# Optimization experiments

Hardware: AMD Instinct MI355X
Metric: run time of the kernel (lower is better)

The kernel has to match this reference:

```python
import jax, jax.numpy as jnp
import numpy as np

B, C, H, W = 8, 256, 64, 64
HID = 4 * C          # mlp_ratio = 4
M = C // 8           # KAttention scale = 8
EPS = 1e-6


def setup_inputs() -> dict:
    key = jax.random.key(0)
    ks = jax.random.split(key, 24)
    n = lambda k, s, sc=1.0: jax.random.normal(k, s, dtype=jnp.float32) * sc
    return {
        "x": n(ks[0], (B, C, H, W)),
        "y": n(ks[1], (B, C, H, W)),
        # shared SeparableConvBN(dim, dim, k=3): 1x1 conv -> depthwise 3x3 -> BN(eval, folded to scale/shift)
        "conv_pw_w": n(ks[2], (C, C), 0.05),
        "conv_dw_w": n(ks[3], (C, 1, 3, 3), 0.1),
        "conv_bn_s": 1.0 + n(ks[4], (C,), 0.1),
        "conv_bn_t": n(ks[5], (C,), 0.1),
        # shared BatchNorm2d(dim) `self.norm` (eval mode, folded)
        "norm_s": 1.0 + n(ks[6], (C,), 0.1),
        "norm_t": n(ks[7], (C,), 0.1),
        # KAttention 1x1 convs (no bias) + gamma
        "q_w": n(ks[8], (M, C), 0.05),
        "k_w": n(ks[9], (M, C), 0.05),
        "v_w": n(ks[10], (C, C), 0.05),
        "gamma_k": n(ks[11], (1,), 0.1),
        # CAttention gamma
        "gamma_c": n(ks[12], (1,), 0.1),
        # Mlp: ConvBN(1x1, bias) -> ReLU6 -> ConvBN(1x1, bias); dropout = identity (eval)
        "fc1_w": n(ks[13], (HID, C), 0.05),
        "fc1_b": n(ks[14], (HID,), 0.05),
        "bn1_s": 1.0 + n(ks[15], (HID,), 0.1),
        "bn1_t": n(ks[16], (HID,), 0.1),
        "fc2_w": n(ks[17], (C, HID), 0.05),
        "fc2_b": n(ks[18], (C,), 0.05),
        "bn2_s": 1.0 + n(ks[19], (C,), 0.1),
        "bn2_t": n(ks[20], (C,), 0.1),
    }


def _bn(x, s, t):
    return x * s[None, :, None, None] + t[None, :, None, None]


def _c1(x, w, b=None):
    # 1x1 conv as channel matmul: [B,C,H,W] x [O,C] -> [B,O,H,W]
    out = jnp.einsum('bchw,oc->bohw', x, w)
    return out if b is None else out + b[None, :, None, None]


def _dw3(x, w):
    # depthwise 3x3, padding=1
    return jax.lax.conv_general_dilated(
        x, w, window_strides=(1, 1), padding='SAME',
        feature_group_count=x.shape[1],
        dimension_numbers=('NCHW', 'OIHW', 'NCHW'))


def reference(x, y, conv_pw_w, conv_dw_w, conv_bn_s, conv_bn_t, norm_s, norm_t,
              q_w, k_w, v_w, gamma_k, gamma_c,
              fc1_w, fc1_b, bn1_s, bn1_t, fc2_w, fc2_b, bn2_s, bn2_t):

    def sepconvbn(z):
        return _bn(_dw3(_c1(z, conv_pw_w), conv_dw_w), conv_bn_s, conv_bn_t)

    def norm(z):
        return _bn(z, norm_s, norm_t)

    def katt(z):
        b, c, h, w = z.shape
        N = h * w
        Q = jax.nn.softplus(_c1(z, q_w)).reshape(b, M, N).transpose(0, 2, 1)  # [b,N,m]
        K = jax.nn.softplus(_c1(z, k_w)).reshape(b, M, N)                    # [b,m,N]
        V = _c1(z, v_w).reshape(b, c, N)                                     # [b,c,N]
        KV = jnp.einsum('bmn,bcn->bmc', K, V)                                # [b,m,c]
        inv = 1.0 / jnp.einsum('bnm,bm->bn', Q, K.sum(-1) + EPS)            # [b,N]
        wv = jnp.einsum('bnm,bmc,bn->bcn', Q, KV, inv)                       # [b,c,N]
        return z + gamma_k[0] * wv.reshape(b, c, h, w)

    def catt(z):
        b, c, h, w = z.shape
        f = z.reshape(b, c, h * w)
        energy = jnp.einsum('bcn,bdn->bcd', f, f)                            # [b,c,c]
        att = jax.nn.softmax(energy.max(-1, keepdims=True) - energy, axis=-1)
        out = jnp.einsum('bcd,bdn->bcn', att, f).reshape(b, c, h, w)
        return gamma_c[0] * out + z

    def light(z):
        return katt(z) + catt(z)

    def mlp(z):
        hdn = jnp.clip(_bn(_c1(z, fc1_w, fc1_b), bn1_s, bn1_t), 0.0, 6.0)  # ReLU6
        return _bn(_c1(hdn, fc2_w, fc2_b), bn2_s, bn2_t)

    x1 = norm(sepconvbn(x))
    ax1 = light(x1)
    y1 = norm(sepconvbn(y))
    ay1 = light(y1)
    x2 = mlp(norm(x1 * ay1))
    y2 = mlp(norm(y1 * ax1))
    y3 = y + y2
    x3 = x + x2 + y3
    return (x3, y3)
```

## Files before the change

### kernel.cpp

```cpp
#include <hip/hip_runtime.h>
#include <hip/hip_bf16.h>
#include <math.h>

typedef __hip_bfloat16 bf16;
typedef unsigned short u16;
#define DEV __device__ __forceinline__

DEV float tofl(float v){ return v; }
DEV bf16  f2b(float v){ return __float2bfloat16(v); }
DEV u16   f2bu(float v){ bf16 h = f2b(v); u16 u; __builtin_memcpy(&u,&h,2); return u; }
DEV float u2f(u16 u){ bf16 h; __builtin_memcpy(&h,&u,2); return __bfloat162float(h); }

static constexpr int Cc=256, Nn=4096, Mm=32;
static constexpr size_t ACT = (size_t)8*Cc*Nn;
static constexpr float EPSc = 1e-6f;

typedef __attribute__((ext_vector_type(8))) __bf16 bf16x8;
typedef __attribute__((ext_vector_type(4))) float  f32x4;

struct StageRegs { int4 a[4], b[4]; };

DEV void stage_load(const u16* __restrict__ gA, int ldA,
                    const u16* __restrict__ gB, int ldB, int tid, StageRegs& r)
{
  int row = tid>>3, g = tid&7;
#pragma unroll
  for(int i=0;i<4;i++){
    r.a[i] = *(const int4*)(gA + (size_t)(row+32*i)*ldA + g*8);
    r.b[i] = *(const int4*)(gB + (size_t)(row+32*i)*ldB + g*8);
  }
}
DEV void stage_write(u16* __restrict__ sA, u16* __restrict__ sB,
                     int tid, const StageRegs& r)
{
  int row = tid>>3, g = tid&7;
#pragma unroll
  for(int i=0;i<4;i++){
    int rr = row+32*i;
    int gg = ((g ^ (rr&7))<<3);
    *(int4*)(sA + rr*64 + gg) = r.a[i];
    *(int4*)(sB + rr*64 + gg) = r.b[i];
  }
}

template<int KDIM, int OMODE>
__global__ __launch_bounds__(256,2) void gemm_bf16(
    const u16* __restrict__ A, long sAb,
    const u16* __restrict__ B,
    float* __restrict__ Cf, u16* __restrict__ Cb,
    const float* __restrict__ bia, const float* __restrict__ scl,
    const float* __restrict__ sht)
{
  __shared__ __align__(16) u16 sA[2][8192];
  __shared__ __align__(16) u16 sB[2][8192];
  int tid = threadIdx.x;
  int nt = blockIdx.x, mt = blockIdx.y, b = blockIdx.z;
  const u16* gA = A + (size_t)b*sAb + (size_t)mt*128*KDIM;
  const u16* gB = B + ((size_t)b*4096 + (size_t)nt*128)*KDIM;
  int w = tid>>6, l = tid&63;
  int wr = w>>1, wc = w&1;
  int l15 = l&15, lg = l>>4;
  f32x4 acc[4][4] = {};
  StageRegs r;
  stage_load(gA, KDIM, gB, KDIM, tid, r);
  stage_write(sA[0], sB[0], tid, r);
  __syncthreads();
  constexpr int NT = KDIM/64;
  for(int t=0;t<NT;t++){
    int cur = t&1;
    if(t+1<NT) stage_load(gA + (t+1)*64, KDIM, gB + (t+1)*64, KDIM, tid, r);
#pragma unroll
    for(int ks=0;ks<2;ks++){
      bf16x8 af[4], bfr[4];
#pragma unroll
      for(int m=0;m<4;m++){
        int row = wr*64 + m*16 + l15;
        int g = ks*4 + lg;
        af[m] = *(const bf16x8*)(&sA[cur][row*64 + ((g^(row&7))<<3)]);
      }
#pragma unroll
      for(int nn=0;nn<4;nn++){
        int row = wc*64 + nn*16 + l15;
        int g = ks*4 + lg;
        bfr[nn] = *(const bf16x8*)(&sB[cur][row*64 + ((g^(row&7))<<3)]);
      }
#pragma unroll
      for(int m=0;m<4;m++)
#pragma unroll
        for(int nn=0;nn<4;nn++)
          acc[m][nn] = __builtin_amdgcn_mfma_f32_16x16x32_bf16(af[m], bfr[nn], acc[m][nn], 0,0,0);
    }
    if(t+1<NT) stage_write(sA[cur^1], sB[cur^1], tid, r);
    __syncthreads();
  }
  int obase = mt*128 + wr*64;
  int nbase = nt*128 + wc*64;
  if (OMODE==0){
    size_t Mrows = (size_t)gridDim.y*128;
#pragma unroll
    for(int m=0;m<4;m++)
#pragma unroll
      for(int nn=0;nn<4;nn++){
        int o_ = obase + m*16 + (lg<<2);
        int n_ = nbase + nn*16 + l15;
        float* dst = Cf + (((size_t)b*Mrows + o_)<<12) + n_;
#pragma unroll
        for(int i=0;i<4;i++) dst[(size_t)i<<12] = acc[m][nn][i];
      }
  } else if (OMODE==1){
#pragma unroll
    for(int m=0;m<4;m++)
#pragma unroll
      for(int nn=0;nn<4;nn++){
        int o_ = obase + m*16 + (lg<<2);
        int n_ = nbase + nn*16 + l15;
        union { u16 u[4]; uint2 v; } pk;
#pragma unroll
        for(int i=0;i<4;i++){
          int o = o_+i;
          float a2 = (acc[m][nn][i] + bia[o])*scl[o] + sht[o];
          pk.u[i] = f2bu(fminf(fmaxf(a2,0.f),6.f));
        }
        *(uint2*)(Cb + ((size_t)b*4096 + (size_t)n_)*1024 + o_) = pk.v;
      }
  } else {
    size_t Mrows = (size_t)gridDim.y*128;
#pragma unroll
    for(int m=0;m<4;m++)
#pragma unroll
      for(int nn=0;nn<4;nn++){
        int o_ = obase + m*16 + (lg<<2);
        int n_ = nbase + nn*16 + l15;
        u16* dst = Cb + (((size_t)b*Mrows + o_)<<12) + n_;
#pragma unroll
        for(int i=0;i<4;i++) dst[(size_t)i<<12] = f2bu(acc[m][nn][i]);
      }
  }
}

__global__ __launch_bounds__(256,2) void qk_gemm(
    const u16* __restrict__ Aqk, const u16* __restrict__ B,
    float* __restrict__ Qf, float* __restrict__ Kf, u16* __restrict__ Kb)
{
  __shared__ __align__(16) u16 sA[2][8192];
  __shared__ __align__(16) u16 sB[2][8192];
  int tid = threadIdx.x;
  int nt = blockIdx.x, b = blockIdx.z;
  const u16* gA = Aqk;
  const u16* gB = B + ((size_t)b*4096 + (size_t)nt*128)*256;
  int w = tid>>6, l = tid&63;
  int wr = w>>1, wc = w&1;
  int l15 = l&15, lg = l>>4;
  f32x4 acc[4][4] = {};
  StageRegs r;
  stage_load(gA, 256, gB, 256, tid, r);
  stage_write(sA[0], sB[0], tid, r);
  __syncthreads();
  for(int t=0;t<4;t++){
    int cur = t&1;
    if(t+1<4) stage_load(gA + (t+1)*64, 256, gB + (t+1)*64, 256, tid, r);
#pragma unroll
    for(int ks=0;ks<2;ks++){
      bf16x8 af[4], bfr[4];
#pragma unroll
      for(int m=0;m<4;m++){
        int row = wr*64 + m*16 + l15;
        int g = ks*4 + lg;
        af[m] = *(const bf16x8*)(&sA[cur][row*64 + ((g^(row&7))<<3)]);
      }
#pragma unroll
      for(int nn=0;nn<4;nn++){
        int row = wc*64 + nn*16 + l15;
        int g = ks*4 + lg;
        bfr[nn] = *(const bf16x8*)(&sB[cur][row*64 + ((g^(row&7))<<3)]);
      }
#pragma unroll
      for(int m=0;m<4;m++)
#pragma unroll
        for(int nn=0;nn<4;nn++)
          acc[m][nn] = __builtin_amdgcn_mfma_f32_16x16x32_bf16(af[m], bfr[nn], acc[m][nn], 0,0,0);
    }
    if(t+1<4) stage_write(sA[cur^1], sB[cur^1], tid, r);
    __syncthreads();
  }
  if (wr!=0) return;
  int nbase = nt*128 + wc*64;
#pragma unroll
  for(int m=0;m<4;m++)
#pragma unroll
    for(int nn=0;nn<4;nn++){
      int o_ = m*16 + (lg<<2);
      int n_ = nbase + nn*16 + l15;
#pragma unroll
      for(int i=0;i<4;i++){
        float a = acc[m][nn][i];
        a = fmaxf(a,0.f) + log1pf(expf(-fabsf(a)));
        if (m<2){
          Qf[(((size_t)b*32 + o_+i)<<12) + n_] = a;
        } else {
          int kr = o_+i-32;
          Kf[(((size_t)b*32 + kr)<<12) + n_] = a;
          Kb[(((size_t)b*32 + kr)<<12) + n_] = f2bu(a);
        }
      }
    }
}

__global__ __launch_bounds__(256,2) void kv_gemm(const u16* __restrict__ Kb,
    const u16* __restrict__ Vb, float* __restrict__ Cp)
{
  __shared__ __align__(16) u16 sA[2][8192];
  __shared__ __align__(16) u16 sB[2][8192];
  int tid = threadIdx.x;
  int nt = blockIdx.x;
  int b  = blockIdx.z >> 4, ks = blockIdx.z & 15;
  const u16* gA = Kb + ((size_t)b*32)*4096 + ks*256;
  const u16* gB = Vb + ((size_t)b*256 + (size_t)nt*128)*4096 + ks*256;
  int row = tid>>3, g = tid&7;
  int w = tid>>6, l = tid&63;
  int wr = w>>1, wc = w&1;
  int l15 = l&15, lg = l>>4;
  f32x4 acc[4][4] = {};
  StageRegs r;
#define KV_LOAD(koff) do { \
    _Pragma("unroll") \
    for(int i=0;i<4;i++){ \
      r.a[i] = *(const int4*)(gA + (size_t)row*4096 + (koff) + g*8); \
      r.b[i] = *(const int4*)(gB + (size_t)(row+32*i)*4096 + (koff) + g*8); \
    } } while(0)
  KV_LOAD(0);
  stage_write(sA[0], sB[0], tid, r);
  __syncthreads();
  for(int t=0;t<4;t++){
    int cur = t&1;
    if(t+1<4) KV_LOAD((t+1)*64);
#pragma unroll
    for(int kss=0;kss<2;kss++){
      bf16x8 af[4], bfr[4];
#pragma unroll
      for(int m=0;m<4;m++){
        int rr = wr*64 + m*16 + l15;
        int gg = kss*4 + lg;
        af[m] = *(const bf16x8*)(&sA[cur][rr*64 + ((gg^(rr&7))<<3)]);
      }
#pragma unroll
      for(int nn=0;nn<4;nn++){
        int rr = wc*64 + nn*16 + l15;
        int gg = kss*4 + lg;
        bfr[nn] = *(const bf16x8*)(&sB[cur][rr*64 + ((gg^(rr&7))<<3)]);
      }
#pragma unroll
      for(int m=0;m<4;m++)
#pragma unroll
        for(int nn=0;nn<4;nn++)
          acc[m][nn] = __builtin_amdgcn_mfma_f32_16x16x32_bf16(af[m], bfr[nn], acc[m][nn], 0,0,0);
    }
    if(t+1<4) stage_write(sA[cur^1], sB[cur^1], tid, r);
    __syncthreads();
  }
#undef KV_LOAD
  if (wr!=0) return;
  float* Cb = Cp + ((size_t)ks*8 + b)*8192;
#pragma unroll
  for(int m=0;m<2;m++)
#pragma unroll
    for(int nn=0;nn<4;nn++){
      int o_ = m*16 + (lg<<2);
      int c_ = nt*128 + wc*64 + nn*16 + l15;
#pragma unroll
      for(int i=0;i<4;i++) Cb[(size_t)(o_+i)*256 + c_] = acc[m][nn][i];
    }
}

__global__ __launch_bounds__(256) void kv_combine16(const float* __restrict__ p,
    float* __restrict__ o)
{
  int i = blockIdx.x*256 + threadIdx.x;
  float s = 0.f;
#pragma unroll
  for(int ks=0;ks<16;ks++) s += p[(size_t)ks*65536 + i];
  o[i] = s;
}

template<int KTILES, int KSPLIT, int OMODE>
__global__ __launch_bounds__(256,2) void gemm3(
    const u16* __restrict__ Ah, const u16* __restrict__ Al, int ldA, long sAb,
    const u16* __restrict__ Bh, const u16* __restrict__ Bl, int ldB, long sBb,
    float* __restrict__ Cf)
{
  __shared__ __align__(16) u16 sA[2][8192];
  __shared__ __align__(16) u16 sB[2][8192];
  int tid = threadIdx.x;
  int nt = blockIdx.x, mt = blockIdx.y;
  int b  = blockIdx.z / KSPLIT, ks = blockIdx.z % KSPLIT;
  long koff = (long)ks * (KTILES*64);
  const u16* A0 = Ah + (size_t)b*sAb + (size_t)mt*128*ldA + koff;
  const u16* A1 = Al + (size_t)b*sAb + (size_t)mt*128*ldA + koff;
  const u16* B0 = Bh + (size_t)b*sBb + (size_t)nt*128*ldB + koff;
  const u16* B1 = Bl + (size_t)b*sBb + (size_t)nt*128*ldB + koff;
  int w = tid>>6, l = tid&63;
  int wr = w>>1, wc = w&1;
  int l15 = l&15, lg = l>>4;
  f32x4 acc[4][4] = {};
  StageRegs r;
  for(int pass=0; pass<3; ++pass){
    const u16* gA = (pass==2) ? A1 : A0;
    const u16* gB = (pass==1) ? B1 : B0;
    stage_load(gA, ldA, gB, ldB, tid, r);
    stage_write(sA[0], sB[0], tid, r);
    __syncthreads();
    for(int t=0;t<KTILES;t++){
      int cur = t&1;
      if(t+1<KTILES) stage_load(gA + (t+1)*64, ldA, gB + (t+1)*64, ldB, tid, r);
#pragma unroll
      for(int kss=0;kss<2;kss++){
        bf16x8 af[4], bfr[4];
#pragma unroll
        for(int m=0;m<4;m++){
          int row = wr*64 + m*16 + l15;
          int g = kss*4 + lg;
          af[m] = *(const bf16x8*)(&sA[cur][row*64 + ((g^(row&7))<<3)]);
        }
#pragma unroll
        for(int nn=0;nn<4;nn++){
          int row = wc*64 + nn*16 + l15;
          int g = kss*4 + lg;
          bfr[nn] = *(const bf16x8*)(&sB[cur][row*64 + ((g^(row&7))<<3)]);
        }
#pragma unroll
        for(int m=0;m<4;m++)
#pragma unroll
          for(int nn=0;nn<4;nn++)
            acc[m][nn] = __builtin_amdgcn_mfma_f32_16x16x32_bf16(af[m], bfr[nn], acc[m][nn], 0,0,0);
      }
      if(t+1<KTILES) stage_write(sA[cur^1], sB[cur^1], tid, r);
      __syncthreads();
    }
  }
  int obase = mt*128 + wr*64;
  int nbase = nt*128 + wc*64;
  if (OMODE==0){
    size_t Mrows = (size_t)gridDim.y*128;
#pragma unroll
    for(int m=0;m<4;m++)
#pragma unroll
      for(int nn=0;nn<4;nn++){
        int o_ = obase + m*16 + (lg<<2);
        int n_ = nbase + nn*16 + l15;
        float* dst = Cf + (((size_t)b*Mrows + o_)<<12) + n_;
#pragma unroll
        for(int i=0;i<4;i++) dst[(size_t)i<<12] = acc[m][nn][i];
      }
  } else {
    int gridB = gridDim.z / KSPLIT;
    float* Cb = Cf + ((size_t)ks*gridB + b)*65536;
#pragma unroll
    for(int m=0;m<4;m++)
#pragma unroll
      for(int nn=0;nn<4;nn++){
        int o_ = obase + m*16 + (lg<<2);
        int n_ = nbase + nn*16 + l15;
#pragma unroll
        for(int i=0;i<4;i++) Cb[(size_t)(o_+i)*256 + n_] = acc[m][nn][i];
      }
  }
}

__global__ __launch_bounds__(256) void cvt_w(const float* __restrict__ s,
    u16* __restrict__ d)
{
  int i = blockIdx.x*256 + threadIdx.x;
  d[i] = f2bu(s[i]);
}
__global__ __launch_bounds__(256) void cvt_wsplit(const float* __restrict__ s,
    u16* __restrict__ dh, u16* __restrict__ dl)
{
  int i = blockIdx.x*256 + threadIdx.x;
  float v = s[i];
  u16 h = f2bu(v);
  dh[i] = h; dl[i] = f2bu(v - u2f(h));
}
__global__ __launch_bounds__(256) void cvt_qk(const float* __restrict__ q,
    const float* __restrict__ k, u16* __restrict__ A)
{
  int r = blockIdx.x, c = threadIdx.x;
  float v = 0.f;
  if (r < 32) v = q[r*256 + c];
  else if (r < 64) v = k[(r-32)*256 + c];
  A[r*256 + c] = f2bu(v);
}
__global__ __launch_bounds__(256) void cvt_split_nm(const float* __restrict__ x,
    u16* __restrict__ xh, u16* __restrict__ xl)
{
  int n  = blockIdx.x*256 + threadIdx.x;
  int c0 = blockIdx.y*16;
  int b  = blockIdx.z;
  union { u16 u[16]; uint4 q[2]; } ph, pl;
#pragma unroll
  for (int oo=0;oo<16;oo++){
    float v = x[(((size_t)b*256 + c0 + oo)<<12) + n];
    u16 h = f2bu(v);
    ph.u[oo] = h; pl.u[oo] = f2bu(v - u2f(h));
  }
  size_t o = (((size_t)b*4096 + n)<<8) + c0;
  *(uint4*)(xh+o) = ph.q[0]; *(uint4*)(xh+o+8) = ph.q[1];
  *(uint4*)(xl+o) = pl.q[0]; *(uint4*)(xl+o+8) = pl.q[1];
}
__global__ __launch_bounds__(256) void cvt_transpose(const u16* __restrict__ zc,
    u16* __restrict__ zn)
{
  int n  = blockIdx.x*256 + threadIdx.x;
  int c0 = blockIdx.y*16;
  int b  = blockIdx.z;
  union { u16 u[16]; uint4 q[2]; } pk;
#pragma unroll
  for (int oo=0;oo<16;oo++)
    pk.u[oo] = zc[(((size_t)b*256 + c0 + oo)<<12) + n];
  u16* dst = zn + (((size_t)b*4096 + n)<<8) + c0;
  *(uint4*)dst       = pk.q[0];
  *(uint4*)(dst + 8) = pk.q[1];
}

__global__ __launch_bounds__(256) void dw_norm_tile(const float* __restrict__ pw,
    u16* __restrict__ zh, u16* __restrict__ zl, const float* __restrict__ dww,
    const float* __restrict__ cbs, const float* __restrict__ cbt,
    const float* __restrict__ ns, const float* __restrict__ nt)
{
  int bc = blockIdx.x;
  int c = bc & 255;
  __shared__ float sp[66*66];
  int tid = threadIdx.x;
  if (tid < 66){ sp[tid] = 0.f; sp[65*66 + tid] = 0.f; }
  if (tid >= 128 && tid < 192) sp[(tid-128+1)*66] = 0.f;
  if (tid >= 192)              sp[(tid-192+1)*66 + 65] = 0.f;
  const float* src = pw + ((size_t)bc << 12);
#pragma unroll
  for(int it=0; it<4; it++){
    int idx = tid + it*256;
    int r = idx >> 4, c4 = idx & 15;
    float4 v = *(const float4*)(src + (idx<<2));
    float* d = &sp[(r+1)*66 + 1 + (c4<<2)];
    d[0]=v.x; d[1]=v.y; d[2]=v.z; d[3]=v.w;
  }
  __syncthreads();
  const float* wp = dww + c*9;
  float w00=wp[0], w01=wp[1], w02=wp[2],
        w10=wp[3], w11=wp[4], w12=wp[5],
        w20=wp[6], w21=wp[7], w22=wp[8];
  float sc = cbs[c]*ns[c];
  float sh = cbt[c]*ns[c] + nt[c];
  int r  = tid >> 2;
  int c0 = (tid & 3) << 4;
  const float* row0 = &sp[r*66 + c0];
  const float* row1 = row0 + 66;
  const float* row2 = row1 + 66;
  union { u16 u[16]; uint4 q[2]; } ph, pl;
#pragma unroll
  for(int j=0;j<16;j++){
    float acc = w00*row0[j] + w01*row0[j+1] + w02*row0[j+2]
              + w10*row1[j] + w11*row1[j+1] + w12*row1[j+2]
              + w20*row2[j] + w21*row2[j+1] + w22*row2[j+2];
    float v = acc*sc + sh;
    u16 hi = f2bu(v);
    ph.u[j] = hi; pl.u[j] = f2bu(v - u2f(hi));
  }
  size_t o = ((size_t)bc << 12) + (r<<6) + c0;
  *(uint4*)(zh+o)   = ph.q[0]; *(uint4*)(zh+o+8) = ph.q[1];
  *(uint4*)(zl+o)   = pl.q[0]; *(uint4*)(zl+o+8) = pl.q[1];
}

__global__ __launch_bounds__(256) void softmax16(const float* __restrict__ Ep,
    u16* __restrict__ att)
{
  int bc = blockIdx.x;
  int b = bc>>8, c = bc&255;
  size_t base = (size_t)b*65536 + (size_t)c*256;
  int d = threadIdx.x;
  float ed = 0.f;
#pragma unroll
  for(int ks=0;ks<16;ks++) ed += Ep[base + (size_t)ks*524288 + d];
  __shared__ float red[4];
  int lane = d&63, wid = d>>6;
  float v = ed;
  for (int off=32;off;off>>=1) v = fmaxf(v, __shfl_down(v,off));
  if(lane==0) red[wid]=v;
  __syncthreads();
  float rowmax = fmaxf(fmaxf(red[0],red[1]),fmaxf(red[2],red[3]));
  __syncthreads();
  float s = rowmax - ed;
  float v2 = s;
  for (int off=32;off;off>>=1) v2 = fmaxf(v2, __shfl_down(v2,off));
  if(lane==0) red[wid]=v2;
  __syncthreads();
  float smax = fmaxf(fmaxf(red[0],red[1]),fmaxf(red[2],red[3]));
  __syncthreads();
  float p = expf(s - smax);
  float sv = p;
  for (int off=32;off;off>>=1) sv += __shfl_down(sv,off);
  if(lane==0) red[wid]=sv;
  __syncthreads();
  float sum = red[0]+red[1]+red[2]+red[3];
  att[((size_t)bc<<8)+d] = f2bu(p/sum);
}

__global__ __launch_bounds__(256) void catt_px(const u16* __restrict__ zh,
    const u16* __restrict__ zl, const u16* __restrict__ oh,
    const u16* __restrict__ ol, const float* __restrict__ Qf,
    const float* __restrict__ KVf, const float* __restrict__ invb,
    const u16* __restrict__ s1b, const float* __restrict__ gkp,
    const float* __restrict__ gcp, const float* __restrict__ ns,
    const float* __restrict__ nt, u16* __restrict__ px)
{
  int n  = blockIdx.x*256 + threadIdx.x;
  int c0 = blockIdx.y*16;
  int b  = blockIdx.z;
  const float* qb  = Qf  + (((size_t)b*Mm)<<12) + n;
  const float* kvb = KVf + ((size_t)b<<13) + c0;
  float s2[16] = {};
#pragma unroll
  for (int m=0;m<Mm;m++){
    float qm = qb[(size_t)m<<12];
#pragma unroll
    for (int oo=0;oo<16;oo++) s2[oo] = fmaf(qm, kvb[m*256 + oo], s2[oo]);
  }
  float invv = invb[((size_t)b<<12)+n];
  float gk = gkp[0], gc = gcp[0];
  union { u16 u[16]; uint4 q[2]; } pk;
#pragma unroll
  for (int oo=0;oo<16;oo++){
    int c = c0+oo;
    size_t idx = (((size_t)b*256 + c)<<12) + n;
    float zv = u2f(zh[idx]) + u2f(zl[idx]);
    float ov = u2f(oh[idx]) + u2f(ol[idx]);
    float a = 2.f*zv + gc*u2f(s1b[idx]) + gk*s2[oo]*invv;
    pk.u[oo] = f2bu(ov*a*ns[c] + nt[c]);
  }
  u16* dst = px + (((size_t)b*4096 + n)<<8) + c0;
  *(uint4*)dst       = pk.q[0];
  *(uint4*)(dst + 8) = pk.q[1];
}

__global__ __launch_bounds__(256) void rowsum_lit(const float* __restrict__ A, float* __restrict__ out)
{
  int x = blockIdx.x;
  const float* ar = A + ((size_t)x << 12);
  float a = 0.f;
  for(int n=threadIdx.x; n<Nn; n+=256) a += ar[n];
  __shared__ float red[4];
  for(int off=32;off;off>>=1) a += __shfl_down(a,off);
  int lane = threadIdx.x&63, wid = threadIdx.x>>6;
  if(lane==0) red[wid]=a;
  __syncthreads();
  if(threadIdx.x==0) out[x] = red[0]+red[1]+red[2]+red[3];
}

__global__ __launch_bounds__(256) void inv_lit(const float* __restrict__ Qf,
    const float* __restrict__ Ks, float* __restrict__ invb)
{
  size_t idx = (size_t)blockIdx.x*256 + threadIdx.x;
  int b = (int)(idx>>12);
  const float* qb = Qf + ((size_t)b*Mm << 12) + (int)(idx&4095);
  const float* ks = Ks + b*Mm;
  float s = 0.f;
  for(int m=0;m<Mm;m++) s += qb[(size_t)m<<12]*(ks[m]+EPSc);
  invb[idx] = 1.f/s;
}

__global__ __launch_bounds__(256) void final_y(const float* __restrict__ yin,
    const float* __restrict__ acc, const float* __restrict__ b2,
    const float* __restrict__ s2, const float* __restrict__ t2, float* __restrict__ out)
{
  size_t idx = (size_t)blockIdx.x*256 + threadIdx.x;
  int c = (int)((idx>>12) & 255);
  float y2 = (acc[idx] + b2[c])*s2[c] + t2[c];
  out[ACT + idx] = yin[idx] + y2;
}

__global__ __launch_bounds__(256) void final_x(const float* __restrict__ xin,
    const float* __restrict__ acc, const float* __restrict__ b2,
    const float* __restrict__ s2, const float* __restrict__ t2, float* __restrict__ out)
{
  size_t idx = (size_t)blockIdx.x*256 + threadIdx.x;
  int c = (int)((idx>>12) & 255);
  float x2 = (acc[idx] + b2[c])*s2[c] + t2[c];
  out[idx] = xin[idx] + x2 + out[ACT + idx];
}

extern "C" void kernel_launch(void* const* d_in, const int* in_sizes, int n_in,
                              void* d_out, int out_size, void* d_ws, size_t ws_size,
                              hipStream_t stream)
{
  (void)in_sizes; (void)n_in; (void)out_size; (void)ws_size;
  const float* xin  = (const float*)d_in[0];
  const float* yin  = (const float*)d_in[1];
  const float* pw_w = (const float*)d_in[2];
  const float* dw_w = (const float*)d_in[3];
  const float* cbs  = (const float*)d_in[4];
  const float* cbt  = (const float*)d_in[5];
  const float* ns   = (const float*)d_in[6];
  const float* nt   = (const float*)d_in[7];
  const float* q_w  = (const float*)d_in[8];
  const float* k_w  = (const float*)d_in[9];
  const float* v_w  = (const float*)d_in[10];
  const float* gk   = (const float*)d_in[11];
  const float* gc   = (const float*)d_in[12];
  const float* fc1_w= (const float*)d_in[13];
  const float* fc1_b= (const float*)d_in[14];
  const float* bn1s = (const float*)d_in[15];
  const float* bn1t = (const float*)d_in[16];
  const float* fc2_w= (const float*)d_in[17];
  const float* fc2_b= (const float*)d_in[18];
  const float* bn2s = (const float*)d_in[19];
  const float* bn2t = (const float*)d_in[20];

  char* ws = (char*)d_ws;
  u16*   Vb    = (u16*)  (ws);
  float* KVp   = (float*)(ws + 16777216);
  u16*   Kb    = (u16*)  (ws + 20971520);
  float* Ep    = (float*)(ws);
  u16*   s1b16 = (u16*)  (ws);
  float* accb  = (float*)(ws);
  float* Apw   = (float*)(ws);
  u16*   x1h   = (u16*)  (ws + 33554432);
  u16*   x1l   = (u16*)  (ws + 50331648);
  u16*   y1h   = (u16*)  (ws + 67108864);
  u16*   y1l   = (u16*)  (ws + 83886080);
  u16*   hid   = (u16*)  (ws + 33554432);
  u16*   px_y  = (u16*)  (ws + 100663296);
  u16*   px_x  = (u16*)  (ws + 117440512);
  u16*   xh_nm = (u16*)  (ws + 100663296);
  u16*   xl_nm = (u16*)  (ws + 117440512);
  u16*   z1b   = (u16*)  (ws + 117440512);
  float* Qf    = (float*)(ws + 134217728);
  float* Kf    = (float*)(ws + 138412032);
  u16*   pwh   = (u16*)  (ws + 134217728);
  u16*   pwl   = (u16*)  (ws + 134217728 + 131072);
  u16*   attb  = (u16*)  (ws + 142606336);
  u16*   fc1wb = (u16*)  (ws + 142606336);
  u16*   fc2wb = (u16*)  (ws + 142606336 + 524288);
  float* KVf   = (float*)(ws + 143654912);
  float* Ksf   = (float*)(ws + 143917056);
  float* invb  = (float*)(ws + 143918080);
  u16*   vwb   = (u16*)  (ws + 144049152);
  u16*   Aqk   = (u16*)  (ws + 144049152 + 131072);

  dim3 blk(256);
  dim3 gPX(16,16,8);
  dim3 gPW(32,2,8), gEn(2,2,128), gG256(32,2,8), gQKg(32,1,8), gKVg(2,1,128);
  dim3 gFC1(32,8,8), gFC2(32,2,8);

  cvt_w<<<dim3(256),blk,0,stream>>>(v_w, vwb);
  cvt_qk<<<dim3(128),blk,0,stream>>>(q_w, k_w, Aqk);

  cvt_wsplit<<<dim3(256),blk,0,stream>>>(pw_w, pwh, pwl);
  for (int im=0;im<2;im++){
    const float* in = (im==0) ? xin : yin;
    u16* zh = (im==0) ? x1h : y1h;
    u16* zl = (im==0) ? x1l : y1l;
    cvt_split_nm<<<gPX,blk,0,stream>>>(in, xh_nm, xl_nm);
    gemm3<4,1,0><<<gPW,blk,0,stream>>>(pwh, pwl, 256, 0,
                                       xh_nm, xl_nm, 256, 1048576, Apw);
    dw_norm_tile<<<dim3(2048),blk,0,stream>>>(Apw, zh, zl, dw_w, cbs, cbt, ns, nt);
  }

  for (int t=0;t<2;t++){
    const u16* zh = (t==0) ? x1h : y1h;
    const u16* zl = (t==0) ? x1l : y1l;
    const u16* oh = (t==0) ? y1h : x1h;
    const u16* ol = (t==0) ? y1l : x1l;
    u16* pxout    = (t==0) ? px_y : px_x;
    cvt_transpose<<<gPX,blk,0,stream>>>(zh, z1b);
    qk_gemm<<<gQKg,blk,0,stream>>>(Aqk, z1b, Qf, Kf, Kb);
    gemm_bf16<256,3><<<gG256,blk,0,stream>>>(vwb, 0, z1b, nullptr, Vb,
                                             nullptr, nullptr, nullptr);
    kv_gemm<<<gKVg,blk,0,stream>>>(Kb, Vb, KVp);
    kv_combine16<<<dim3(256),blk,0,stream>>>(KVp, KVf);
    rowsum_lit<<<dim3(256),blk,0,stream>>>(Kf, Ksf);
    inv_lit<<<dim3(128),blk,0,stream>>>(Qf, Ksf, invb);
    gemm3<4,16,2><<<gEn,blk,0,stream>>>(zh, zl, 4096, 1048576,
                                        zh, zl, 4096, 1048576, Ep);
    softmax16<<<dim3(2048),blk,0,stream>>>(Ep, attb);
    gemm_bf16<256,3><<<gG256,blk,0,stream>>>(attb, 65536, z1b, nullptr, s1b16,
                                             nullptr, nullptr, nullptr);
    catt_px<<<gPX,blk,0,stream>>>(zh, zl, oh, ol, Qf, KVf, invb, s1b16,
                                  gk, gc, ns, nt, pxout);
  }

  cvt_w<<<dim3(1024),blk,0,stream>>>(fc1_w, fc1wb);
  cvt_w<<<dim3(1024),blk,0,stream>>>(fc2_w, fc2wb);
  for (int s=0;s<2;s++){
    const u16* px = (s==0) ? px_y : px_x;
    gemm_bf16<256,1><<<gFC1,blk,0,stream>>>(fc1wb, 0, px, nullptr, hid,
                                            fc1_b, bn1s, bn1t);
    gemm_bf16<1024,0><<<gFC2,blk,0,stream>>>(fc2wb, 0, hid, accb, nullptr,
                                             nullptr, nullptr, nullptr);
    if (s==0) final_y<<<dim3(32768),blk,0,stream>>>(yin, accb, fc2_b, bn2s, bn2t, (float*)d_out);
    else      final_x<<<dim3(32768),blk,0,stream>>>(xin, accb, fc2_b, bn2s, bn2t, (float*)d_out);
  }
}
```

Before: 693.3 us.

## Fuse MLP fc1/fc2/epilogue into one kernel and exploit Gram symmetry

Replaces the two MLP GEMMs and the final elementwise kernels with one fused kernel per stream. It keeps the hidden activations in shared memory, so the bf16 hidden tensor and the fp32 accumulator never go to global memory, and the bias/BN/residual epilogue is applied in place. It also replaces the channel-energy GEMM with a symmetric variant that computes only three of the four 128x128 tiles and writes the off-diagonal tile transposed. Risks are low occupancy: the MLP kernel uses about 112KB of shared memory at one block per CU with a grid of 512 blocks, and fc2 weights are reloaded from global for every block.

```diff
diff --git a/kernel.cpp b/kernel.cpp
--- a/kernel.cpp
+++ b/kernel.cpp
@@ -106,22 +106,6 @@
         float* dst = Cf + (((size_t)b*Mrows + o_)<<12) + n_;
 #pragma unroll
         for(int i=0;i<4;i++) dst[(size_t)i<<12] = acc[m][nn][i];
-      }
-  } else if (OMODE==1){
-#pragma unroll
-    for(int m=0;m<4;m++)
-#pragma unroll
-      for(int nn=0;nn<4;nn++){
-        int o_ = obase + m*16 + (lg<<2);
-        int n_ = nbase + nn*16 + l15;
-        union { u16 u[4]; uint2 v; } pk;
-#pragma unroll
-        for(int i=0;i<4;i++){
-          int o = o_+i;
-          float a2 = (acc[m][nn][i] + bia[o])*scl[o] + sht[o];
-          pk.u[i] = f2bu(fminf(fmaxf(a2,0.f),6.f));
-        }
-        *(uint2*)(Cb + ((size_t)b*4096 + (size_t)n_)*1024 + o_) = pk.v;
       }
   } else {
     size_t Mrows = (size_t)gridDim.y*128;
@@ -366,6 +350,196 @@
   }
 }
 
+__global__ __launch_bounds__(256,2) void gemm3_sym(
+    const u16* __restrict__ Zh, const u16* __restrict__ Zl,
+    float* __restrict__ Cf)
+{
+  __shared__ __align__(16) u16 sA[2][8192];
+  __shared__ __align__(16) u16 sB[2][8192];
+  int tid = threadIdx.x;
+  int pair = blockIdx.x;
+  int nt = (pair==0) ? 0 : (pair==1 ? 1 : 0);
+  int mt = (pair==0) ? 0 : 1;
+  int b  = blockIdx.z >> 4, ks = blockIdx.z & 15;
+  long koff = (long)ks * 256;
+  const u16* A0 = Zh + (size_t)b*1048576 + (size_t)mt*128*4096 + koff;
+  const u16* A1 = Zl + (size_t)b*1048576 + (size_t)mt*128*4096 + koff;
+  const u16* B0 = Zh + (size_t)b*1048576 + (size_t)nt*128*4096 + koff;
+  const u16* B1 = Zl + (size_t)b*1048576 + (size_t)nt*128*4096 + koff;
+  int w = tid>>6, l = tid&63;
+  int wr = w>>1, wc = w&1;
+  int l15 = l&15, lg = l>>4;
+  f32x4 acc[4][4] = {};
+  StageRegs r;
+  for(int pass=0; pass<3; ++pass){
+    const u16* gA = (pass==2) ? A1 : A0;
+    const u16* gB = (pass==1) ? B1 : B0;
+    stage_load(gA, 4096, gB, 4096, tid, r);
+    stage_write(sA[0], sB[0], tid, r);
+    __syncthreads();
+    for(int t=0;t<4;t++){
+      int cur = t&1;
+      if(t+1<4) stage_load(gA + (t+1)*64, 4096, gB + (t+1)*64, 4096, tid, r);
+#pragma unroll
+      for(int kss=0;kss<2;kss++){
+        bf16x8 af[4], bfr[4];
+#pragma unroll
+        for(int m=0;m<4;m++){
+          int row = wr*64 + m*16 + l15;
+          int g = kss*4 + lg;
+          af[m] = *(const bf16x8*)(&sA[cur][row*64 + ((g^(row&7))<<3)]);
+        }
+#pragma unroll
+        for(int nn=0;nn<4;nn++){
+          int row = wc*64 + nn*16 + l15;
+          int g = kss*4 + lg;
+          bfr[nn] = *(const bf16x8*)(&sB[cur][row*64 + ((g^(row&7))<<3)]);
+        }
+#pragma unroll
+        for(int m=0;m<4;m++)
+#pragma unroll
+          for(int nn=0;nn<4;nn++)
+            acc[m][nn] = __builtin_amdgcn_mfma_f32_16x16x32_bf16(af[m], bfr[nn], acc[m][nn], 0,0,0);
+      }
+      if(t+1<4) stage_write(sA[cur^1], sB[cur^1], tid, r);
+      __syncthreads();
+    }
+  }
+  float* Cb = Cf + ((size_t)ks*8 + b)*65536;
+  int obase = mt*128 + wr*64;
+  int nbase = nt*128 + wc*64;
+#pragma unroll
+  for(int m=0;m<4;m++)
+#pragma unroll
+    for(int nn=0;nn<4;nn++){
+      int o_ = obase + m*16 + (lg<<2);
+      int n_ = nbase + nn*16 + l15;
+#pragma unroll
+      for(int i=0;i<4;i++) Cb[(size_t)(o_+i)*256 + n_] = acc[m][nn][i];
+      if (pair==2){
+        float4 v = { acc[m][nn][0], acc[m][nn][1], acc[m][nn][2], acc[m][nn][3] };
+        *(float4*)&Cb[(size_t)n_*256 + o_] = v;
+      }
+    }
+}
+
+template<int FIN>
+__global__ __launch_bounds__(256,1) void mlp_fused(
+    const u16* __restrict__ px, const u16* __restrict__ w1b,
+    const u16* __restrict__ w2b,
+    const float* __restrict__ b1, const float* __restrict__ s1,
+    const float* __restrict__ t1, const float* __restrict__ b2,
+    const float* __restrict__ s2, const float* __restrict__ t2,
+    const float* __restrict__ zin, float* __restrict__ out)
+{
+  __shared__ __align__(16) u16 sPx[64*256];
+  __shared__ __align__(16) u16 sW1[128*256];
+  __shared__ __align__(16) u16 sH [64*128];
+  int tid = threadIdx.x;
+  int n0 = blockIdx.x*64, b = blockIdx.z;
+  int w = tid>>6, l = tid&63, l15 = l&15, lg = l>>4;
+  const u16* gpx = px + (((size_t)b*4096 + n0)<<8);
+#pragma unroll
+  for(int i=0;i<8;i++){
+    int flat = tid + i*256;
+    int row = flat>>5, g = flat&31;
+    *(int4*)&sPx[row*256 + ((g ^ (row&7))<<3)] = *(const int4*)(gpx + row*256 + g*8);
+  }
+  f32x4 acc[4][4] = {};
+  int cw = w*64, hw = w*32;
+  for(int q=0;q<4;q++)
+  for(int hh=0;hh<2;hh++){
+    int hq = q*256 + hh*128;
+    const u16* gw1 = w1b + (size_t)hq*256;
+#pragma unroll
+    for(int i=0;i<16;i++){
+      int flat = tid + i*256;
+      int row = flat>>5, g = flat&31;
+      *(int4*)&sW1[row*256 + ((g ^ (row&7))<<3)] = *(const int4*)(gw1 + row*256 + g*8);
+    }
+    __syncthreads();
+    f32x4 a1[2][4] = {};
+#pragma unroll
+    for(int kst=0;kst<8;kst++){
+      bf16x8 af[2], bfr[4];
+#pragma unroll
+      for(int mi=0;mi<2;mi++){
+        int row = hw + mi*16 + l15;
+        int g = kst*4 + lg;
+        af[mi] = *(const bf16x8*)&sW1[row*256 + ((g^(row&7))<<3)];
+      }
+#pragma unroll
+      for(int nn=0;nn<4;nn++){
+        int row = nn*16 + l15;
+        int g = kst*4 + lg;
+        bfr[nn] = *(const bf16x8*)&sPx[row*256 + ((g^(row&7))<<3)];
+      }
+#pragma unroll
+      for(int mi=0;mi<2;mi++)
+#pragma unroll
+        for(int nn=0;nn<4;nn++)
+          a1[mi][nn] = __builtin_amdgcn_mfma_f32_16x16x32_bf16(af[mi], bfr[nn], a1[mi][nn], 0,0,0);
+    }
+    int4 w2r[4][4];
+#pragma unroll
+    for(int kst=0;kst<4;kst++)
+#pragma unroll
+      for(int mi=0;mi<4;mi++){
+        int row = cw + mi*16 + l15;
+        w2r[kst][mi] = *(const int4*)(w2b + (size_t)row*1024 + hq + kst*32 + lg*8);
+      }
+#pragma unroll
+    for(int mi=0;mi<2;mi++)
+#pragma unroll
+      for(int nn=0;nn<4;nn++){
+        int n_ = nn*16 + l15;
+        int hbase = hw + mi*16 + (lg<<2);
+        int ho = hq + hbase;
+        union{ u16 u[4]; uint2 v; } pk;
+#pragma unroll
+        for(int i=0;i<4;i++){
+          float a2 = (a1[mi][nn][i] + b1[ho+i])*s1[ho+i] + t1[ho+i];
+          pk.u[i] = f2bu(fminf(fmaxf(a2,0.f),6.f));
+        }
+        int o8 = hbase>>2;
+        *(uint2*)&sH[n_*128 + ((o8 ^ ((n_&7)<<1))<<2)] = pk.v;
+      }
+    __syncthreads();
+#pragma unroll
+    for(int kst=0;kst<4;kst++){
+      bf16x8 bfr[4];
+#pragma unroll
+      for(int nn=0;nn<4;nn++){
+        int n_ = nn*16 + l15;
+        int o8 = kst*8 + lg*2;
+        bfr[nn] = *(const bf16x8*)&sH[n_*128 + ((o8 ^ ((n_&7)<<1))<<2)];
+      }
+#pragma unroll
+      for(int mi=0;mi<4;mi++){
+        union { int4 i4; bf16x8 h8; } cvt; cvt.i4 = w2r[kst][mi];
+#pragma unroll
+        for(int nn=0;nn<4;nn++)
+          acc[mi][nn] = __builtin_amdgcn_mfma_f32_16x16x32_bf16(cvt.h8, bfr[nn], acc[mi][nn], 0,0,0);
+      }
+    }
+  }
+#pragma unroll
+  for(int mi=0;mi<4;mi++)
+#pragma unroll
+    for(int nn=0;nn<4;nn++){
+      int co = cw + mi*16 + (lg<<2);
+      int n_ = n0 + nn*16 + l15;
+#pragma unroll
+      for(int i=0;i<4;i++){
+        int c = co+i;
+        size_t idx = (((size_t)b*256 + c)<<12) + n_;
+        float v = (acc[mi][nn][i] + b2[c])*s2[c] + t2[c];
+        if (FIN==0) out[ACT+idx] = zin[idx] + v;
+        else        out[idx]     = zin[idx] + v + out[ACT+idx];
+      }
+    }
+}
+
 __global__ __launch_bounds__(256) void cvt_w(const float* __restrict__ s,
     u16* __restrict__ d)
 {
@@ -564,26 +738,6 @@
   float s = 0.f;
   for(int m=0;m<Mm;m++) s += qb[(size_t)m<<12]*(ks[m]+EPSc);
   invb[idx] = 1.f/s;
-}
-
-__global__ __launch_bounds__(256) void final_y(const float* __restrict__ yin,
-    const float* __restrict__ acc, const float* __restrict__ b2,
-    const float* __restrict__ s2, const float* __restrict__ t2, float* __restrict__ out)
-{
-  size_t idx = (size_t)blockIdx.x*256 + threadIdx.x;
-  int c = (int)((idx>>12) & 255);
-  float y2 = (acc[idx] + b2[c])*s2[c] + t2[c];
-  out[ACT + idx] = yin[idx] + y2;
-}
-
-__global__ __launch_bounds__(256) void final_x(const float* __restrict__ xin,
-    const float* __restrict__ acc, const float* __restrict__ b2,
-    const float* __restrict__ s2, const float* __restrict__ t2, float* __restrict__ out)
-{
-  size_t idx = (size_t)blockIdx.x*256 + threadIdx.x;
-  int c = (int)((idx>>12) & 255);
-  float x2 = (acc[idx] + b2[c])*s2[c] + t2[c];
-  out[idx] = xin[idx] + x2 + out[ACT + idx];
 }
 
 extern "C" void kernel_launch(void* const* d_in, const int* in_sizes, int n_in,
@@ -619,13 +773,11 @@
   u16*   Kb    = (u16*)  (ws + 20971520);
   float* Ep    = (float*)(ws);
   u16*   s1b16 = (u16*)  (ws);
-  float* accb  = (float*)(ws);
   float* Apw   = (float*)(ws);
   u16*   x1h   = (u16*)  (ws + 33554432);
   u16*   x1l   = (u16*)  (ws + 50331648);
   u16*   y1h   = (u16*)  (ws + 67108864);
   u16*   y1l   = (u16*)  (ws + 83886080);
-  u16*   hid   = (u16*)  (ws + 33554432);
   u16*   px_y  = (u16*)  (ws + 100663296);
   u16*   px_x  = (u16*)  (ws + 117440512);
   u16*   xh_nm = (u16*)  (ws + 100663296);
@@ -646,8 +798,8 @@
 
   dim3 blk(256);
   dim3 gPX(16,16,8);
-  dim3 gPW(32,2,8), gEn(2,2,128), gG256(32,2,8), gQKg(32,1,8), gKVg(2,1,128);
-  dim3 gFC1(32,8,8), gFC2(32,2,8);
+  dim3 gPW(32,2,8), gEn(3,1,128), gG256(32,2,8), gQKg(32,1,8), gKVg(2,1,128);
+  dim3 gMLP(64,1,8);
 
   cvt_w<<<dim3(256),blk,0,stream>>>(v_w, vwb);
   cvt_qk<<<dim3(128),blk,0,stream>>>(q_w, k_w, Aqk);
@@ -677,8 +829,7 @@
     kv_combine16<<<dim3(256),blk,0,stream>>>(KVp, KVf);
     rowsum_lit<<<dim3(256),blk,0,stream>>>(Kf, Ksf);
     inv_lit<<<dim3(128),blk,0,stream>>>(Qf, Ksf, invb);
-    gemm3<4,16,2><<<gEn,blk,0,stream>>>(zh, zl, 4096, 1048576,
-                                        zh, zl, 4096, 1048576, Ep);
+    gemm3_sym<<<gEn,blk,0,stream>>>(zh, zl, Ep);
     softmax16<<<dim3(2048),blk,0,stream>>>(Ep, attb);
     gemm_bf16<256,3><<<gG256,blk,0,stream>>>(attb, 65536, z1b, nullptr, s1b16,
                                              nullptr, nullptr, nullptr);
@@ -688,13 +839,8 @@
 
   cvt_w<<<dim3(1024),blk,0,stream>>>(fc1_w, fc1wb);
   cvt_w<<<dim3(1024),blk,0,stream>>>(fc2_w, fc2wb);
-  for (int s=0;s<2;s++){
-    const u16* px = (s==0) ? px_y : px_x;
-    gemm_bf16<256,1><<<gFC1,blk,0,stream>>>(fc1wb, 0, px, nullptr, hid,
-                                            fc1_b, bn1s, bn1t);
-    gemm_bf16<1024,0><<<gFC2,blk,0,stream>>>(fc2wb, 0, hid, accb, nullptr,
-                                             nullptr, nullptr, nullptr);
-    if (s==0) final_y<<<dim3(32768),blk,0,stream>>>(yin, accb, fc2_b, bn2s, bn2t, (float*)d_out);
-    else      final_x<<<dim3(32768),blk,0,stream>>>(xin, accb, fc2_b, bn2s, bn2t, (float*)d_out);
-  }
-}
+  mlp_fused<0><<<gMLP,blk,0,stream>>>(px_y, fc1wb, fc2wb, fc1_b, bn1s, bn1t,
+                                      fc2_b, bn2s, bn2t, yin, (float*)d_out);
+  mlp_fused<1><<<gMLP,blk,0,stream>>>(px_x, fc1wb, fc2wb, fc1_b, bn1s, bn1t,
+                                      fc2_b, bn2s, bn2t, xin, (float*)d_out);
+}
```

After: 710.6 us. 1.02x slower.
